# Kernel optimization log

Hardware: AMD Instinct MI355X
Metric: run time of the kernel (lower is better)

## Reference

```python
import jax, jax.numpy as jnp
import numpy as np

ROUTING_ITERS = 3
EPS = 1e-8


def squash(x):
    # scale = ||x||^2 / (1 + ||x||^2); out = scale * x / (||x|| + eps)
    norm = jnp.linalg.norm(x, axis=-1, keepdims=True)
    scale = norm ** 2 / (1.0 + norm ** 2)
    return scale * x / (norm + EPS)


def setup_inputs() -> dict:
    key = jax.random.key(0)
    kx, kw = jax.random.split(key)
    B, R, C, IC, OC = 256, 1152, 10, 8, 16
    x = jax.random.normal(kx, (B, R, IC), dtype=jnp.float32)
    # learned prediction weights: [1, num_routes, num_capsules, in_ch, out_ch]
    weights = jax.random.normal(kw, (1, R, C, IC, OC), dtype=jnp.float32)
    return {"x": x, "weights": weights}


def reference(x, weights):
    # prediction vectors u_hat[b,r,c,o] = sum_i x[b,r,i] * W[r,c,i,o]
    u = jnp.einsum('bri,rcio->brco', x, weights[0])  # [B,R,C,OC]
    b = jnp.zeros(u.shape[:3], dtype=u.dtype)        # routing logits [B,R,C]
    v = jnp.zeros(u.shape[:1] + u.shape[2:], dtype=u.dtype)
    for _ in range(ROUTING_ITERS):
        c = jax.nn.softmax(b, axis=-1)               # coupling coeffs over capsules
        s = jnp.einsum('brc,brco->bco', c, u)        # weighted sum over routes
        v = squash(s)                                # [B,C,OC]
        b = b + jnp.einsum('brco,bco->brc', u, v)    # agreement update
    return v
```

## Files before the change

### kernel.cpp

```cpp
#include <hip/hip_runtime.h>
#include <cstdint>
#include <cstddef>

#define NB 256
#define NR 1152
#define NC 10
#define NI 8
#define NO 16
#define NSPLIT 2
#define NSWEEP 9
#define NRC 144

static __device__ __forceinline__ uint32_t bf16_pack2(float lo, float hi) {
    uint32_t vl = __float_as_uint(lo);
    vl = vl + 0x7FFFu + ((vl >> 16) & 1u);
    uint32_t vh = __float_as_uint(hi);
    vh = vh + 0x7FFFu + ((vh >> 16) & 1u);
    return (vl >> 16) | (vh & 0xFFFF0000u);
}

__global__ __launch_bounds__(320, 2) void caps_u_s1_kernel(
    const float* __restrict__ x, const float* __restrict__ W,
    uint32_t* __restrict__ u, float* __restrict__ part1)
{
    const int t  = threadIdx.x;
    const int c  = t >> 5;
    const int rl = (t & 31) >> 2;
    const int oq = t & 3;
    const int rc = blockIdx.x >> 4;
    const int bg = blockIdx.x & 15;
    const int b0 = bg * 16;
    const int r  = rc * 8 + rl;

    __shared__ float xs[16][8][8];

    if (t < 256) {
        const int bi = t >> 4, rem = t & 15;
        const int rr = rem >> 1, hf = rem & 1;
        *(float4*)&xs[bi][rr][hf * 4] =
            *(const float4*)(x + ((size_t)(b0 + bi) * NR + rc * 8 + rr) * 8 + hf * 4);
    }

    const float* wb = W + ((size_t)r * NC + c) * (NI * NO) + oq * 4;
    float4 wf[8];
#pragma unroll
    for (int i = 0; i < 8; ++i) wf[i] = *(const float4*)(wb + i * NO);

    __syncthreads();

#pragma unroll 2
    for (int bi = 0; bi < 16; ++bi) {
        const float4 xv4a = *(const float4*)&xs[bi][rl][0];
        const float4 xv4b = *(const float4*)&xs[bi][rl][4];
        const float xr[8] = {xv4a.x, xv4a.y, xv4a.z, xv4a.w,
                             xv4b.x, xv4b.y, xv4b.z, xv4b.w};
        float ax = 0.f, ay = 0.f, az = 0.f, aw = 0.f;
#pragma unroll
        for (int i = 0; i < 8; ++i) {
            const float xv = xr[i];
            ax = fmaf(xv, wf[i].x, ax); ay = fmaf(xv, wf[i].y, ay);
            az = fmaf(xv, wf[i].z, az); aw = fmaf(xv, wf[i].w, aw);
        }
        uint2 s;
        s.x = bf16_pack2(ax, ay);
        s.y = bf16_pack2(az, aw);
        *(uint2*)(u + (((size_t)(b0 + bi) * NC + c) * NR + r) * 8 + oq * 2) = s;

        float sx = ax, sy = ay, sz = az, sw = aw;
#pragma unroll
        for (int off = 4; off <= 16; off <<= 1) {
            sx += __shfl_xor(sx, off); sy += __shfl_xor(sy, off);
            sz += __shfl_xor(sz, off); sw += __shfl_xor(sw, off);
        }
        if ((t & 28) == 0) {
            const float4 sv = {sx, sy, sz, sw};
            *(float4*)(part1 + (((size_t)(b0 + bi) * NRC + rc) * 160)
                       + c * 16 + oq * 4) = sv;
        }
    }
}

__global__ __launch_bounds__(192) void caps_s1_reduce_kernel(
    const float* __restrict__ part1, float* __restrict__ vsum)
{
    const int b = blockIdx.x;
    const int t = threadIdx.x;
    if (t >= 160) return;
    float s0 = 0.f, s1 = 0.f, s2 = 0.f, s3 = 0.f;
    const float* p = part1 + (size_t)b * NRC * 160 + t;
#pragma unroll 4
    for (int g = 0; g < NRC; g += 4) {
        s0 += p[(g + 0) * 160];
        s1 += p[(g + 1) * 160];
        s2 += p[(g + 2) * 160];
        s3 += p[(g + 3) * 160];
    }
    const float s = 0.1f * ((s0 + s1) + (s2 + s3));
    float n2 = s * s;
    n2 += __shfl_xor(n2, 1);
    n2 += __shfl_xor(n2, 2);
    n2 += __shfl_xor(n2, 4);
    n2 += __shfl_xor(n2, 8);
    const float nrm   = sqrtf(n2);
    const float scale = n2 / (1.f + n2) / (nrm + 1e-8f);
    vsum[(size_t)b * 160 + t] = scale * s;
}

__global__ __launch_bounds__(256, 2) void caps_pass_kernel(
    const uint32_t* __restrict__ u, const float* __restrict__ vsum,
    float* __restrict__ part2)
{
    const int b  = blockIdx.x >> 1;
    const int sp = blockIdx.x & 1;
    const int t  = threadIdx.x;
    const int oq = t & 3;
    const int rl = t >> 2;

    __shared__ float vss[160];
    __shared__ float sred[4][160];

    if (t < 160) vss[t] = vsum[(size_t)b * 160 + t];
    __syncthreads();

    float acc[10][4];
#pragma unroll
    for (int c = 0; c < 10; ++c)
#pragma unroll
        for (int j = 0; j < 4; ++j) acc[c][j] = 0.f;

    const uint2* ub = (const uint2*)u + (size_t)b * NC * NR * 4 + oq;

    for (int k = 0; k < NSWEEP; ++k) {
        const int r = sp * (NSWEEP * 64) + k * 64 + rl;
        uint2 q[10];
#pragma unroll
        for (int c = 0; c < 10; ++c) q[c] = ub[((size_t)c * NR + r) * 4];

        float lg[10];
#pragma unroll
        for (int c = 0; c < 10; ++c) {
            const float4 vq = *(const float4*)&vss[c * 16 + oq * 4];
            float d = __uint_as_float(q[c].x << 16) * vq.x;
            d = fmaf(__uint_as_float(q[c].x & 0xFFFF0000u), vq.y, d);
            d = fmaf(__uint_as_float(q[c].y << 16),         vq.z, d);
            d = fmaf(__uint_as_float(q[c].y & 0xFFFF0000u), vq.w, d);
            lg[c] = d;
        }
#pragma unroll
        for (int c = 0; c < 10; ++c) {
            lg[c] += __shfl_xor(lg[c], 1);
            lg[c] += __shfl_xor(lg[c], 2);
        }
        float m = lg[0];
#pragma unroll
        for (int c = 1; c < 10; ++c) m = fmaxf(m, lg[c]);
        float wgt[10], ssum = 0.f;
#pragma unroll
        for (int c = 0; c < 10; ++c) { wgt[c] = __expf(lg[c] - m); ssum += wgt[c]; }
        const float inv = 1.f / ssum;
#pragma unroll
        for (int c = 0; c < 10; ++c) {
            const float wv = wgt[c] * inv;
            acc[c][0] = fmaf(wv, __uint_as_float(q[c].x << 16),         acc[c][0]);
            acc[c][1] = fmaf(wv, __uint_as_float(q[c].x & 0xFFFF0000u), acc[c][1]);
            acc[c][2] = fmaf(wv, __uint_as_float(q[c].y << 16),         acc[c][2]);
            acc[c][3] = fmaf(wv, __uint_as_float(q[c].y & 0xFFFF0000u), acc[c][3]);
        }
    }

#pragma unroll
    for (int off = 4; off <= 32; off <<= 1)
#pragma unroll
        for (int c = 0; c < 10; ++c)
#pragma unroll
            for (int j = 0; j < 4; ++j) acc[c][j] += __shfl_xor(acc[c][j], off);

    const int wv = t >> 6;
    if ((t & 63) < 4) {
#pragma unroll
        for (int c = 0; c < 10; ++c)
#pragma unroll
            for (int j = 0; j < 4; ++j)
                sred[wv][c * 16 + oq * 4 + j] = acc[c][j];
    }
    __syncthreads();

    if (t < 160) {
        part2[((size_t)sp * NB + b) * 160 + t]
            = sred[0][t] + sred[1][t] + sred[2][t] + sred[3][t];
    }
}

__global__ __launch_bounds__(192) void caps_reduce_kernel(
    const float* __restrict__ part2, float* __restrict__ vsum,
    float* __restrict__ out, const int mode)
{
    const int b = blockIdx.x;
    const int t = threadIdx.x;
    if (t >= 160) return;
    float s = 0.f;
#pragma unroll
    for (int sp = 0; sp < NSPLIT; ++sp)
        s += part2[((size_t)sp * NB + b) * 160 + t];
    float n2 = s * s;
    n2 += __shfl_xor(n2, 1);
    n2 += __shfl_xor(n2, 2);
    n2 += __shfl_xor(n2, 4);
    n2 += __shfl_xor(n2, 8);
    const float nrm   = sqrtf(n2);
    const float scale = n2 / (1.f + n2) / (nrm + 1e-8f);
    const float v = scale * s;
    if (mode == 1) vsum[(size_t)b * 160 + t] += v;
    else           out[(size_t)b * 160 + t] = v;
}

extern "C" void kernel_launch(void* const* d_in, const int* in_sizes, int n_in,
                              void* d_out, int out_size, void* d_ws, size_t ws_size,
                              hipStream_t stream) {
    const float* x = (const float*)d_in[0];
    const float* W = (const float*)d_in[1];
    float* out = (float*)d_out;

    uint8_t*  ws   = (uint8_t*)d_ws;
    uint32_t* u    = (uint32_t*)ws;
    float*    prt1 = (float*)(ws + 94371840u);
    float*    prt2 = (float*)(ws + 94371840u + 23592960u);
    float*    vsm  = (float*)(ws + 94371840u + 23592960u + 327680u);

    caps_u_s1_kernel     <<<2304, 320, 0, stream>>>(x, W, u, prt1);
    caps_s1_reduce_kernel<<<NB, 192, 0, stream>>>(prt1, vsm);
    caps_pass_kernel     <<<NB * NSPLIT, 256, 0, stream>>>(u, vsm, prt2);
    caps_reduce_kernel   <<<NB, 192, 0, stream>>>(prt2, vsm, nullptr, 1);
    caps_pass_kernel     <<<NB * NSPLIT, 256, 0, stream>>>(u, vsm, prt2);
    caps_reduce_kernel   <<<NB, 192, 0, stream>>>(prt2, nullptr, out, 2);
}
```

Measured before the change: 141.6 us.

## Fuse reduce kernels into pass kernel prologue and store stage-1 partials as bf16

New measurement: 142.8 us. About the same (+0.8%).

```diff
diff --git a/kernel.cpp b/kernel.cpp
--- a/kernel.cpp
+++ b/kernel.cpp
@@ -21,7 +21,7 @@
 
 __global__ __launch_bounds__(320, 2) void caps_u_s1_kernel(
     const float* __restrict__ x, const float* __restrict__ W,
-    uint32_t* __restrict__ u, float* __restrict__ part1)
+    uint32_t* __restrict__ u, uint32_t* __restrict__ part1)
 {
     const int t  = threadIdx.x;
     const int c  = t >> 5;
@@ -73,27 +73,31 @@
             sz += __shfl_xor(sz, off); sw += __shfl_xor(sw, off);
         }
         if ((t & 28) == 0) {
-            const float4 sv = {sx, sy, sz, sw};
-            *(float4*)(part1 + (((size_t)(b0 + bi) * NRC + rc) * 160)
-                       + c * 16 + oq * 4) = sv;
-        }
-    }
-}
-
-__global__ __launch_bounds__(192) void caps_s1_reduce_kernel(
-    const float* __restrict__ part1, float* __restrict__ vsum)
-{
-    const int b = blockIdx.x;
-    const int t = threadIdx.x;
-    if (t >= 160) return;
+            uint2 p;
+            p.x = bf16_pack2(sx, sy);
+            p.y = bf16_pack2(sz, sw);
+            *(uint2*)(part1 + ((size_t)(b0 + bi) * NRC + rc) * 80
+                      + c * 8 + oq * 2) = p;
+        }
+    }
+}
+
+static __device__ __forceinline__ float vsum1_col(
+    const uint32_t* __restrict__ part1, const int b, const int t)
+{
+    const uint32_t* p = part1 + (size_t)b * NRC * 80 + (t >> 1);
+    const bool hi = t & 1;
     float s0 = 0.f, s1 = 0.f, s2 = 0.f, s3 = 0.f;
-    const float* p = part1 + (size_t)b * NRC * 160 + t;
 #pragma unroll 4
     for (int g = 0; g < NRC; g += 4) {
-        s0 += p[(g + 0) * 160];
-        s1 += p[(g + 1) * 160];
-        s2 += p[(g + 2) * 160];
-        s3 += p[(g + 3) * 160];
+        const uint32_t w0 = p[(g + 0) * 80];
+        const uint32_t w1 = p[(g + 1) * 80];
+        const uint32_t w2 = p[(g + 2) * 80];
+        const uint32_t w3 = p[(g + 3) * 80];
+        s0 += hi ? __uint_as_float(w0 & 0xFFFF0000u) : __uint_as_float(w0 << 16);
+        s1 += hi ? __uint_as_float(w1 & 0xFFFF0000u) : __uint_as_float(w1 << 16);
+        s2 += hi ? __uint_as_float(w2 & 0xFFFF0000u) : __uint_as_float(w2 << 16);
+        s3 += hi ? __uint_as_float(w3 & 0xFFFF0000u) : __uint_as_float(w3 << 16);
     }
     const float s = 0.1f * ((s0 + s1) + (s2 + s3));
     float n2 = s * s;
@@ -102,13 +106,12 @@
     n2 += __shfl_xor(n2, 4);
     n2 += __shfl_xor(n2, 8);
     const float nrm   = sqrtf(n2);
-    const float scale = n2 / (1.f + n2) / (nrm + 1e-8f);
-    vsum[(size_t)b * 160 + t] = scale * s;
+    return s * (n2 / (1.f + n2) / (nrm + 1e-8f));
 }
 
 __global__ __launch_bounds__(256, 2) void caps_pass_kernel(
-    const uint32_t* __restrict__ u, const float* __restrict__ vsum,
-    float* __restrict__ part2)
+    const uint32_t* __restrict__ u, const uint32_t* __restrict__ part1,
+    const float* __restrict__ part_prev, float* __restrict__ partout)
 {
     const int b  = blockIdx.x >> 1;
     const int sp = blockIdx.x & 1;
@@ -119,7 +122,21 @@
     __shared__ float vss[160];
     __shared__ float sred[4][160];
 
-    if (t < 160) vss[t] = vsum[(size_t)b * 160 + t];
+    if (t < 160) {
+        float v = vsum1_col(part1, b, t);
+        if (part_prev != nullptr) {
+            const float s = part_prev[(size_t)b * 160 + t]
+                          + part_prev[((size_t)NB + b) * 160 + t];
+            float n2 = s * s;
+            n2 += __shfl_xor(n2, 1);
+            n2 += __shfl_xor(n2, 2);
+            n2 += __shfl_xor(n2, 4);
+            n2 += __shfl_xor(n2, 8);
+            const float nrm = sqrtf(n2);
+            v += s * (n2 / (1.f + n2) / (nrm + 1e-8f));
+        }
+        vss[t] = v;
+    }
     __syncthreads();
 
     float acc[10][4];
@@ -186,22 +203,19 @@
     __syncthreads();
 
     if (t < 160) {
-        part2[((size_t)sp * NB + b) * 160 + t]
+        partout[((size_t)sp * NB + b) * 160 + t]
             = sred[0][t] + sred[1][t] + sred[2][t] + sred[3][t];
     }
 }
 
-__global__ __launch_bounds__(192) void caps_reduce_kernel(
-    const float* __restrict__ part2, float* __restrict__ vsum,
-    float* __restrict__ out, const int mode)
+__global__ __launch_bounds__(192) void caps_final_kernel(
+    const float* __restrict__ part2b, float* __restrict__ out)
 {
     const int b = blockIdx.x;
     const int t = threadIdx.x;
     if (t >= 160) return;
-    float s = 0.f;
-#pragma unroll
-    for (int sp = 0; sp < NSPLIT; ++sp)
-        s += part2[((size_t)sp * NB + b) * 160 + t];
+    const float s = part2b[(size_t)b * 160 + t]
+                  + part2b[((size_t)NB + b) * 160 + t];
     float n2 = s * s;
     n2 += __shfl_xor(n2, 1);
     n2 += __shfl_xor(n2, 2);
@@ -209,9 +223,7 @@
     n2 += __shfl_xor(n2, 8);
     const float nrm   = sqrtf(n2);
     const float scale = n2 / (1.f + n2) / (nrm + 1e-8f);
-    const float v = scale * s;
-    if (mode == 1) vsum[(size_t)b * 160 + t] += v;
-    else           out[(size_t)b * 160 + t] = v;
+    out[(size_t)b * 160 + t] = scale * s;
 }
 
 extern "C" void kernel_launch(void* const* d_in, const int* in_sizes, int n_in,
@@ -223,14 +235,12 @@
 
     uint8_t*  ws   = (uint8_t*)d_ws;
     uint32_t* u    = (uint32_t*)ws;
-    float*    prt1 = (float*)(ws + 94371840u);
-    float*    prt2 = (float*)(ws + 94371840u + 23592960u);
-    float*    vsm  = (float*)(ws + 94371840u + 23592960u + 327680u);
-
-    caps_u_s1_kernel     <<<2304, 320, 0, stream>>>(x, W, u, prt1);
-    caps_s1_reduce_kernel<<<NB, 192, 0, stream>>>(prt1, vsm);
-    caps_pass_kernel     <<<NB * NSPLIT, 256, 0, stream>>>(u, vsm, prt2);
-    caps_reduce_kernel   <<<NB, 192, 0, stream>>>(prt2, vsm, nullptr, 1);
-    caps_pass_kernel     <<<NB * NSPLIT, 256, 0, stream>>>(u, vsm, prt2);
-    caps_reduce_kernel   <<<NB, 192, 0, stream>>>(prt2, nullptr, out, 2);
-}
+    uint32_t* prt1 = (uint32_t*)(ws + 94371840u);
+    float*    p2a  = (float*)(ws + 94371840u + 11796480u);
+    float*    p2b  = (float*)(ws + 94371840u + 11796480u + 327680u);
+
+    caps_u_s1_kernel<<<2304, 320, 0, stream>>>(x, W, u, prt1);
+    caps_pass_kernel<<<NB * NSPLIT, 256, 0, stream>>>(u, prt1, nullptr, p2a);
+    caps_pass_kernel<<<NB * NSPLIT, 256, 0, stream>>>(u, prt1, p2a, p2b);
+    caps_final_kernel<<<NB, 192, 0, stream>>>(p2b, out);
+}
```
